# Optimization experiments

Hardware: AMD Instinct MI355X
Metric: run time of the kernel (lower is better)

## Reference

```python
import jax, jax.numpy as jnp
import numpy as np

CONF_THRES = 0.25
IOU_THRES = 0.45
MAX_ANCHORS = 50
PRE_NMS_TOPK = 2048   # candidate cap, standard fused-NMS trick to bound the IoU matrix
NEG = -1.0e9
NUM_CLASSES = 80
IMG = 640.0


def setup_inputs() -> dict:
    key = jax.random.key(0)
    k1, k2, k3, k4 = jax.random.split(key, 4)
    B, N = 16, 25200
    # realistic xyxy boxes inside a 640x640 image
    cxcy = jax.random.uniform(k1, (B, N, 2), minval=0.0, maxval=IMG)
    wh = jax.random.uniform(k2, (B, N, 2), minval=4.0, maxval=64.0)
    x1y1 = jnp.clip(cxcy - 0.5 * wh, 0.0, IMG)
    x2y2 = jnp.clip(cxcy + 0.5 * wh, 0.0, IMG)
    conf = jax.random.uniform(k3, (B, N, 1))
    cls = jax.random.randint(k4, (B, N, 1), 0, NUM_CLASSES).astype(jnp.float32)
    x = jnp.concatenate([x1y1, x2y2, conf, cls], axis=-1)  # [B, N, 6]
    return {"x": x}


def _box_iou_matrix(boxes):
    # boxes: [K, 4] xyxy -> [K, K] pairwise IoU
    x1, y1, x2, y2 = boxes[:, 0], boxes[:, 1], boxes[:, 2], boxes[:, 3]
    area = jnp.maximum(x2 - x1, 0.0) * jnp.maximum(y2 - y1, 0.0)  # [K]
    iw = jnp.maximum(jnp.minimum(x2[:, None], x2[None, :]) - jnp.maximum(x1[:, None], x1[None, :]), 0.0)
    ih = jnp.maximum(jnp.minimum(y2[:, None], y2[None, :]) - jnp.maximum(y1[:, None], y1[None, :]), 0.0)
    inter = iw * ih
    union = area[:, None] + area[None, :] - inter
    return inter / jnp.maximum(union, 1e-9)


def _nms_single(bx):
    # bx: [N, 6] -> [MAX_ANCHORS, 6], rows padded with -1 (keep_shape semantics)
    scores = bx[:, 4]
    s = jnp.where(scores > CONF_THRES, scores, NEG)  # confidence filter
    top_s, top_i = jax.lax.top_k(s, PRE_NMS_TOPK)     # sort descending by score
    cand = jnp.take(bx, top_i, axis=0)                # [K, 6]
    cvalid = top_s > 0.5 * NEG                        # passed conf filter

    iou = _box_iou_matrix(cand[:, :4])                # [K, K]
    idxs = jnp.arange(PRE_NMS_TOPK)
    # box i may only suppress lower-scored boxes j > i
    suppr_rows = (iou >= IOU_THRES) & (idxs[None, :] > idxs[:, None])

    def step(suppressed, i):
        keep_i = cvalid[i] & jnp.logical_not(suppressed[i])
        suppressed = suppressed | (keep_i & suppr_rows[i])
        return suppressed, keep_i

    _, keep = jax.lax.scan(step, jnp.zeros(PRE_NMS_TOPK, dtype=bool), idxs)

    final_s = jnp.where(keep, cand[:, 4], NEG)
    sel_s, sel_i = jax.lax.top_k(final_s, MAX_ANCHORS)  # top-50 kept boxes by conf
    rows = jnp.take(cand, sel_i, axis=0)                # [50, 6]
    return jnp.where((sel_s > 0.5 * NEG)[:, None], rows, -1.0)


def reference(x):
    # x: [B, N, 6] -> [B, MAX_ANCHORS, 6]
    return jax.vmap(_nms_single)(x)
```

## Files before the change

kernel.cpp:

```cpp
#include <hip/hip_runtime.h>

#define BATCH   16
#define NANCH   25200
#define TPB     1024
#define MAXK    50
#define PRETOPK 2048
#define CONF_T  0.25f
#define IOU_T   0.45f
#define NEGV    -1000000000.0f
#define NBINS   4096
#define CHUNK   256

__device__ __forceinline__ int bin_of(float s) {
    int b = (int)((s - CONF_T) * ((float)NBINS / 0.75f));
    return b > (NBINS - 1) ? (NBINS - 1) : b;
}

__global__ __launch_bounds__(TPB, 1) void nms_kernel(const float* __restrict__ x,
                                                     float* __restrict__ out) {
    __shared__ float s_scores[NANCH];
    __shared__ unsigned int s_hist[NBINS];
    __shared__ unsigned long long s_keys[CHUNK];
    __shared__ float s_srows[CHUNK][8];
    __shared__ float s_kx1[MAXK], s_ky1[MAXK], s_kx2[MAXK], s_ky2[MAXK], s_ka[MAXK];
    __shared__ int s_hi, s_c, s_cnt, s_nk, s_P;

    const int b    = blockIdx.x;
    const int tid  = threadIdx.x;
    const int lane = tid & 63;
    const int wave = tid >> 6;

    const float* __restrict__ xb = x + (size_t)b * NANCH * 6;
    float* __restrict__ ob       = out + (size_t)b * MAXK * 6;

    for (int i = tid; i < NBINS; i += TPB) s_hist[i] = 0u;
    if (tid == 0) { s_hi = NBINS; s_nk = 0; s_P = 0; }
    __syncthreads();

    for (int i = tid; i < NANCH; i += TPB) {
        float s = xb[(size_t)i * 6 + 4];
        bool valid = s > CONF_T;
        s_scores[i] = valid ? s : NEGV;
        if (valid) atomicAdd(&s_hist[bin_of(s)], 1u);
    }
    __syncthreads();

    while (s_nk < MAXK && s_P < PRETOPK && s_hi > 0) {
        if (wave == 0) {
            int c = s_hi;
            int room = CHUNK;
            while (c > 0) {
                int nb = c < 64 ? c : 64;
                unsigned cnt = (lane < nb) ? s_hist[c - 1 - lane] : 0u;
                unsigned pre = cnt;
                #pragma unroll
                for (int o = 1; o < 64; o <<= 1) {
                    unsigned t = __shfl_up(pre, o);
                    if (lane >= o) pre += t;
                }
                unsigned total = __shfl(pre, 63);
                if (total <= (unsigned)room) { room -= (int)total; c -= nb; continue; }
                unsigned long long m = __ballot((lane < nb) && (pre <= (unsigned)room));
                int n = __popcll(m);
                if (n == 0 && room == CHUNK) n = 1;
                c -= n;
                break;
            }
            if (lane == 0) s_c = c;
        } else {
            int z = tid - 64;
            if (z < CHUNK) s_keys[z] = 0ULL;
            if (z == CHUNK) s_cnt = 0;
        }
        __syncthreads();

        const int c = s_c, hi = s_hi;

        for (int i = tid; i < NANCH; i += TPB) {
            float s = s_scores[i];
            if (s > CONF_T) {
                int bn = bin_of(s);
                if (bn >= c && bn < hi) {
                    int slot = atomicAdd(&s_cnt, 1);
                    if (slot < CHUNK) {
                        s_keys[slot] =
                            ((unsigned long long)__float_as_uint(s) << 32) |
                            ((unsigned long long)(65535 - i) << 16) |
                            (unsigned long long)slot;
                    }
                }
            }
        }
        __syncthreads();

        const int K = (s_cnt < CHUNK) ? s_cnt : CHUNK;

        if (tid < CHUNK) {
            const unsigned long long mykey = s_keys[tid];
            float2 r0, r1, r2;
            const bool real = tid < K;
            if (real) {
                int myi = 65535 - (int)((mykey >> 16) & 0xFFFFULL);
                const float2* rp = (const float2*)(xb + (size_t)myi * 6);
                r0 = rp[0]; r1 = rp[1]; r2 = rp[2];
            }
            int r = 0;
            #pragma unroll 4
            for (int j = 0; j < CHUNK; ++j) r += (s_keys[j] > mykey) ? 1 : 0;
            if (real) {
                s_srows[r][0] = r0.x; s_srows[r][1] = r0.y;
                s_srows[r][2] = r1.x; s_srows[r][3] = r1.y;
                s_srows[r][4] = r2.x; s_srows[r][5] = r2.y;
            }
        }
        __syncthreads();

        if (wave == 0) {
            const int rem   = PRETOPK - s_P;
            const int Kproc = K < rem ? K : rem;
            int nk = s_nk;

            for (int tb = 0; tb < Kproc && nk < MAXK; tb += 64) {
                const int lim = (Kproc - tb) < 64 ? (Kproc - tb) : 64;
                float4 bx = {0.f, 0.f, 0.f, 0.f};
                float2 be = {0.f, 0.f};
                bool sup = lane >= lim;
                if (!sup) {
                    bx = *(const float4*)&s_srows[tb + lane][0];
                    be = *(const float2*)&s_srows[tb + lane][4];
                }
                const float ba = fmaxf(bx.z - bx.x, 0.f) * fmaxf(bx.w - bx.y, 0.f);

                for (int j = 0; j < nk; ++j) {
                    float iw = fmaxf(fminf(bx.z, s_kx2[j]) - fmaxf(bx.x, s_kx1[j]), 0.f);
                    float ih = fmaxf(fminf(bx.w, s_ky2[j]) - fmaxf(bx.y, s_ky1[j]), 0.f);
                    float inter = iw * ih;
                    sup = sup || (inter / fmaxf(ba + s_ka[j] - inter, 1e-9f)) >= IOU_T;
                }

                unsigned long long m = 0ULL;
                #pragma unroll 8
                for (int j = 0; j < 64; ++j) {
                    if (j >= lim) break;
                    const float4 oj = *(const float4*)&s_srows[tb + j][0];
                    const float oa = fmaxf(oj.z - oj.x, 0.f) * fmaxf(oj.w - oj.y, 0.f);
                    float iw = fmaxf(fminf(bx.z, oj.z) - fmaxf(bx.x, oj.x), 0.f);
                    float ih = fmaxf(fminf(bx.w, oj.w) - fmaxf(bx.y, oj.y), 0.f);
                    float inter = iw * ih;
                    bool ov = (inter / fmaxf(ba + oa - inter, 1e-9f)) >= IOU_T;
                    m |= ov ? (1ULL << j) : 0ULL;
                }
                m &= ~(1ULL << lane);

                unsigned long long alive = __ballot(!sup);
                unsigned long long keepmask = 0ULL;
                while (alive != 0ULL && nk < MAXK) {
                    const int j = __builtin_ctzll(alive);
                    keepmask |= 1ULL << j;
                    ++nk;
                    const unsigned long long kill = __ballot((m >> j) & 1ULL);
                    alive &= ~(kill | (1ULL << j));
                }

                if ((keepmask >> lane) & 1ULL) {
                    const int nk0 = nk - __popcll(keepmask);
                    const int pos = nk0 + __popcll(keepmask & ((1ULL << lane) - 1ULL));
                    s_kx1[pos] = bx.x; s_ky1[pos] = bx.y;
                    s_kx2[pos] = bx.z; s_ky2[pos] = bx.w; s_ka[pos] = ba;
                    ob[pos * 6 + 0] = bx.x;
                    ob[pos * 6 + 1] = bx.y;
                    ob[pos * 6 + 2] = bx.z;
                    ob[pos * 6 + 3] = bx.w;
                    ob[pos * 6 + 4] = be.x;
                    ob[pos * 6 + 5] = be.y;
                }
            }
            if (lane == 0) { s_nk = nk; s_P = s_P + Kproc; s_hi = s_c; }
        }
        __syncthreads();
    }

    const int nkf = s_nk;
    for (int i = tid; i < (MAXK - nkf) * 6; i += TPB) {
        ob[nkf * 6 + i] = -1.0f;
    }
}

extern "C" void kernel_launch(void* const* d_in, const int* in_sizes, int n_in,
                              void* d_out, int out_size, void* d_ws, size_t ws_size,
                              hipStream_t stream) {
    const float* x = (const float*)d_in[0];
    float* out     = (float*)d_out;
    nms_kernel<<<BATCH, TPB, 0, stream>>>(x, out);
}
```

Before: 28.16 us.

## Replace histogram chunk selection with fixed high-score threshold fast path

Drops the score histogram and the iterative bin-chunk selection loop. A single unrolled pass collects only candidates scoring above a fixed threshold (0.9905) into a 320-entry buffer, rank-sorts them and runs the wavefront NMS once. If that buffer overflows, or fewer than 50 boxes are kept, it falls back to a slow block-wide argmax pop loop. The threshold is tuned to the expected score distribution: results stay correct for any input, but inputs with few high scores would hit the much slower fallback.

```diff
diff --git a/kernel.cpp b/kernel.cpp
--- a/kernel.cpp
+++ b/kernel.cpp
@@ -3,27 +3,24 @@
 #define BATCH   16
 #define NANCH   25200
 #define TPB     1024
+#define NWAVES  (TPB / 64)
 #define MAXK    50
 #define PRETOPK 2048
 #define CONF_T  0.25f
 #define IOU_T   0.45f
 #define NEGV    -1000000000.0f
-#define NBINS   4096
-#define CHUNK   256
-
-__device__ __forceinline__ int bin_of(float s) {
-    int b = (int)((s - CONF_T) * ((float)NBINS / 0.75f));
-    return b > (NBINS - 1) ? (NBINS - 1) : b;
-}
+#define T0      0.9905f
+#define CAP     320
 
 __global__ __launch_bounds__(TPB, 1) void nms_kernel(const float* __restrict__ x,
                                                      float* __restrict__ out) {
     __shared__ float s_scores[NANCH];
-    __shared__ unsigned int s_hist[NBINS];
-    __shared__ unsigned long long s_keys[CHUNK];
-    __shared__ float s_srows[CHUNK][8];
+    __shared__ unsigned long long s_keys[CAP];
+    __shared__ float s_srows[CAP][8];
     __shared__ float s_kx1[MAXK], s_ky1[MAXK], s_kx2[MAXK], s_ky2[MAXK], s_ka[MAXK];
-    __shared__ int s_hi, s_c, s_cnt, s_nk, s_P;
+    __shared__ float s_wval[NWAVES];
+    __shared__ int   s_widx[NWAVES];
+    __shared__ int   s_cnt, s_nk, s_best;
 
     const int b    = blockIdx.x;
     const int tid  = threadIdx.x;
@@ -33,72 +30,54 @@
     const float* __restrict__ xb = x + (size_t)b * NANCH * 6;
     float* __restrict__ ob       = out + (size_t)b * MAXK * 6;
 
-    for (int i = tid; i < NBINS; i += TPB) s_hist[i] = 0u;
-    if (tid == 0) { s_hi = NBINS; s_nk = 0; s_P = 0; }
-    __syncthreads();
-
-    for (int i = tid; i < NANCH; i += TPB) {
-        float s = xb[(size_t)i * 6 + 4];
-        bool valid = s > CONF_T;
-        s_scores[i] = valid ? s : NEGV;
-        if (valid) atomicAdd(&s_hist[bin_of(s)], 1u);
-    }
-    __syncthreads();
-
-    while (s_nk < MAXK && s_P < PRETOPK && s_hi > 0) {
-        if (wave == 0) {
-            int c = s_hi;
-            int room = CHUNK;
-            while (c > 0) {
-                int nb = c < 64 ? c : 64;
-                unsigned cnt = (lane < nb) ? s_hist[c - 1 - lane] : 0u;
-                unsigned pre = cnt;
-                #pragma unroll
-                for (int o = 1; o < 64; o <<= 1) {
-                    unsigned t = __shfl_up(pre, o);
-                    if (lane >= o) pre += t;
-                }
-                unsigned total = __shfl(pre, 63);
-                if (total <= (unsigned)room) { room -= (int)total; c -= nb; continue; }
-                unsigned long long m = __ballot((lane < nb) && (pre <= (unsigned)room));
-                int n = __popcll(m);
-                if (n == 0 && room == CHUNK) n = 1;
-                c -= n;
-                break;
-            }
-            if (lane == 0) s_c = c;
-        } else {
-            int z = tid - 64;
-            if (z < CHUNK) s_keys[z] = 0ULL;
-            if (z == CHUNK) s_cnt = 0;
-        }
-        __syncthreads();
-
-        const int c = s_c, hi = s_hi;
-
-        for (int i = tid; i < NANCH; i += TPB) {
-            float s = s_scores[i];
-            if (s > CONF_T) {
-                int bn = bin_of(s);
-                if (bn >= c && bn < hi) {
+    if (tid < CAP) s_keys[tid] = 0ULL;
+    if (tid == 0) { s_cnt = 0; s_nk = 0; }
+    __syncthreads();
+
+    {
+        int i = tid;
+        for (int c = 0; c < 3; ++c) {
+            float v[8];
+            #pragma unroll
+            for (int k = 0; k < 8; ++k) v[k] = xb[(size_t)(i + k * TPB) * 6 + 4];
+            #pragma unroll
+            for (int k = 0; k < 8; ++k) {
+                const int idx = i + k * TPB;
+                s_scores[idx] = (v[k] > CONF_T) ? v[k] : NEGV;
+                if (v[k] > T0) {
                     int slot = atomicAdd(&s_cnt, 1);
-                    if (slot < CHUNK) {
+                    if (slot < CAP)
                         s_keys[slot] =
-                            ((unsigned long long)__float_as_uint(s) << 32) |
-                            ((unsigned long long)(65535 - i) << 16) |
+                            ((unsigned long long)__float_as_uint(v[k]) << 32) |
+                            ((unsigned long long)(65535 - idx) << 16) |
                             (unsigned long long)slot;
-                    }
-                }
-            }
-        }
-        __syncthreads();
-
-        const int K = (s_cnt < CHUNK) ? s_cnt : CHUNK;
-
-        if (tid < CHUNK) {
+                }
+            }
+            i += 8 * TPB;
+        }
+        if (i < NANCH) {
+            float s = xb[(size_t)i * 6 + 4];
+            s_scores[i] = (s > CONF_T) ? s : NEGV;
+            if (s > T0) {
+                int slot = atomicAdd(&s_cnt, 1);
+                if (slot < CAP)
+                    s_keys[slot] =
+                        ((unsigned long long)__float_as_uint(s) << 32) |
+                        ((unsigned long long)(65535 - i) << 16) |
+                        (unsigned long long)slot;
+            }
+        }
+    }
+    __syncthreads();
+
+    const int cnt   = s_cnt;
+    const bool fast = cnt <= CAP;
+
+    if (fast) {
+        if (tid < CAP) {
             const unsigned long long mykey = s_keys[tid];
             float2 r0, r1, r2;
-            const bool real = tid < K;
+            const bool real = tid < cnt;
             if (real) {
                 int myi = 65535 - (int)((mykey >> 16) & 0xFFFFULL);
                 const float2* rp = (const float2*)(xb + (size_t)myi * 6);
@@ -106,7 +85,7 @@
             }
             int r = 0;
             #pragma unroll 4
-            for (int j = 0; j < CHUNK; ++j) r += (s_keys[j] > mykey) ? 1 : 0;
+            for (int j = 0; j < CAP; ++j) r += (s_keys[j] > mykey) ? 1 : 0;
             if (real) {
                 s_srows[r][0] = r0.x; s_srows[r][1] = r0.y;
                 s_srows[r][2] = r1.x; s_srows[r][3] = r1.y;
@@ -116,12 +95,9 @@
         __syncthreads();
 
         if (wave == 0) {
-            const int rem   = PRETOPK - s_P;
-            const int Kproc = K < rem ? K : rem;
-            int nk = s_nk;
-
-            for (int tb = 0; tb < Kproc && nk < MAXK; tb += 64) {
-                const int lim = (Kproc - tb) < 64 ? (Kproc - tb) : 64;
+            int nk = 0;
+            for (int tb = 0; tb < cnt && nk < MAXK; tb += 64) {
+                const int lim = (cnt - tb) < 64 ? (cnt - tb) : 64;
                 float4 bx = {0.f, 0.f, 0.f, 0.f};
                 float2 be = {0.f, 0.f};
                 bool sup = lane >= lim;
@@ -175,10 +151,88 @@
                     ob[pos * 6 + 5] = be.y;
                 }
             }
-            if (lane == 0) { s_nk = nk; s_P = s_P + Kproc; s_hi = s_c; }
+            if (lane == 0) s_nk = nk;
         }
         __syncthreads();
     }
+
+    const bool cont = fast && (s_nk < MAXK);
+    if (cont) {
+        for (int i = tid; i < NANCH; i += TPB)
+            if (s_scores[i] > T0) s_scores[i] = NEGV;
+    }
+    __syncthreads();
+
+    int budget = 0;
+    if (!fast)     budget = PRETOPK;
+    else if (cont) budget = PRETOPK - cnt;
+
+    if (budget > 0) {
+        int nk = s_nk;
+        for (int pop = 0; pop < budget && nk < MAXK; ++pop) {
+            float bv = NEGV - 1.0f;
+            int   bi = NANCH;
+            for (int i = tid; i < NANCH; i += TPB) {
+                float s = s_scores[i];
+                if (s > bv) { bv = s; bi = i; }
+            }
+            #pragma unroll
+            for (int off = 32; off >= 1; off >>= 1) {
+                float ov = __shfl_down(bv, off);
+                int   oi = __shfl_down(bi, off);
+                if (ov > bv || (ov == bv && oi < bi)) { bv = ov; bi = oi; }
+            }
+            if (lane == 0) { s_wval[wave] = bv; s_widx[wave] = bi; }
+            __syncthreads();
+            if (wave == 0) {
+                bv = (lane < NWAVES) ? s_wval[lane] : (NEGV - 1.0f);
+                bi = (lane < NWAVES) ? s_widx[lane] : NANCH;
+                #pragma unroll
+                for (int off = 32; off >= 1; off >>= 1) {
+                    float ov = __shfl_down(bv, off);
+                    int   oi = __shfl_down(bi, off);
+                    if (ov > bv || (ov == bv && oi < bi)) { bv = ov; bi = oi; }
+                }
+                if (lane == 0) {
+                    s_best = (bv > 0.5f * NEGV) ? bi : -1;
+                    if (s_best >= 0) s_scores[bi] = NEGV - 1.0f;
+                }
+            }
+            __syncthreads();
+            const int best = s_best;
+            if (best < 0) break;
+
+            if (wave == 0) {
+                const float bx1 = xb[(size_t)best * 6 + 0];
+                const float by1 = xb[(size_t)best * 6 + 1];
+                const float bx2 = xb[(size_t)best * 6 + 2];
+                const float by2 = xb[(size_t)best * 6 + 3];
+                const float ba  = fmaxf(bx2 - bx1, 0.0f) * fmaxf(by2 - by1, 0.0f);
+                bool sup = false;
+                if (lane < nk) {
+                    float iw = fmaxf(fminf(bx2, s_kx2[lane]) - fmaxf(bx1, s_kx1[lane]), 0.f);
+                    float ih = fmaxf(fminf(by2, s_ky2[lane]) - fmaxf(by1, s_ky1[lane]), 0.f);
+                    float inter = iw * ih;
+                    float uni   = ba + s_ka[lane] - inter;
+                    sup = (inter / fmaxf(uni, 1e-9f)) >= IOU_T;
+                }
+                if (lane == 0 && __ballot(sup) == 0ULL) {
+                    s_kx1[nk] = bx1; s_ky1[nk] = by1;
+                    s_kx2[nk] = bx2; s_ky2[nk] = by2; s_ka[nk] = ba;
+                    ob[nk * 6 + 0] = bx1;
+                    ob[nk * 6 + 1] = by1;
+                    ob[nk * 6 + 2] = bx2;
+                    ob[nk * 6 + 3] = by2;
+                    ob[nk * 6 + 4] = xb[(size_t)best * 6 + 4];
+                    ob[nk * 6 + 5] = xb[(size_t)best * 6 + 5];
+                    s_nk = nk + 1;
+                }
+            }
+            __syncthreads();
+            nk = s_nk;
+        }
+    }
+    __syncthreads();
 
     const int nkf = s_nk;
     for (int i = tid; i < (MAXK - nkf) * 6; i += TPB) {
```

Result: faster. 25.54 us (-9.3%).
